# Kernel tuning notes

Measured on AMD Instinct MI355X. Metric: run time of the kernel, lower is better.

Reference implementation:

```python
import jax, jax.numpy as jnp
import numpy as np

N_NODES = 50000
N_EDGES = 800000
IN_CH = 384
HID = 128


def _gcn_conv(x, src, dst, W, b, n):
    # PyG GCNConv: h = x @ W; out[dst] += d^-1/2[src] * d^-1/2[dst] * h[src]; out += b
    h = x @ W  # [N, out_ch]
    deg = jax.ops.segment_sum(jnp.ones(src.shape, dtype=h.dtype), dst, num_segments=n)
    dinv = jnp.where(deg > 0, jax.lax.rsqrt(jnp.maximum(deg, 1.0)), 0.0)
    norm = dinv[src] * dinv[dst]  # [E]
    out = jax.ops.segment_sum(h[src] * norm[:, None], dst, num_segments=n)
    return out + b


def setup_inputs() -> dict:
    key = jax.random.key(0)
    k_x, k_e, k1, k2, k3, k4 = jax.random.split(key, 6)
    x = jax.random.normal(k_x, (N_NODES, IN_CH), dtype=jnp.float32)
    edge_index = jax.random.randint(k_e, (2, N_EDGES), 0, N_NODES, dtype=jnp.int64)
    s1 = 1.0 / np.sqrt(IN_CH)
    s2 = 1.0 / np.sqrt(HID)
    W1 = jax.random.uniform(k1, (IN_CH, HID), jnp.float32, -s1, s1)
    b1 = jnp.zeros((HID,), jnp.float32)
    W2 = jax.random.uniform(k2, (HID, HID), jnp.float32, -s2, s2)
    b2 = jnp.zeros((HID,), jnp.float32)
    return {"x": x, "edge_index": edge_index, "W1": W1, "b1": b1, "W2": W2, "b2": b2}


def reference(x, edge_index, W1, b1, W2, b2):
    n = x.shape[0]
    loops = jnp.arange(n, dtype=edge_index.dtype)
    src = jnp.concatenate([edge_index[0], loops])  # add_self_loops
    dst = jnp.concatenate([edge_index[1], loops])
    h = _gcn_conv(x, src, dst, W1, b1, n)
    h = jax.nn.relu(h)  # dropout is identity in eval mode
    out = _gcn_conv(h, src, dst, W2, b2, n)
    return out
```

## Files before the change

### kernel.cpp

```cpp
#include <hip/hip_runtime.h>
#include <hip/hip_fp16.h>

#define NN 50000
#define NE 800000
#define C_IN 384
#define C_HID 128
#define CHK 128
#define ECH 6250
#define NBKT 128
#define BSTR 392

typedef __attribute__((ext_vector_type(8))) short short8;
typedef __attribute__((ext_vector_type(4))) float f32x4;
typedef __attribute__((ext_vector_type(8))) unsigned short us8;

__device__ __forceinline__ ushort f2bf(float x) {
    uint u = __float_as_uint(x);
    uint r = (u + 0x7fffu + ((u >> 16) & 1u)) >> 16;
    return (ushort)r;
}
__device__ __forceinline__ float bf2f(ushort b) { return __uint_as_float(((uint)b) << 16); }

typedef __attribute__((address_space(1))) const unsigned int as1_uint;
typedef __attribute__((address_space(3))) unsigned int as3_uint;
__device__ __forceinline__ void gload16(const void* g, void* l) {
    __builtin_amdgcn_global_load_lds((as1_uint*)g, (as3_uint*)l, 16, 0, 0);
}

__global__ __launch_bounds__(256) void k_hist(const int* __restrict__ dst,
                                              int* __restrict__ histT) {
    __shared__ int h[NBKT];
    const int tid = threadIdx.x;
    if (tid < NBKT) h[tid] = 0;
    __syncthreads();
    const int base = blockIdx.x * ECH;
    for (int i = base + tid; i < base + ECH; i += 256)
        atomicAdd(&h[(uint)dst[i] / BSTR], 1);
    __syncthreads();
    if (tid < NBKT) histT[tid * CHK + blockIdx.x] = h[tid];
}

__global__ __launch_bounds__(1024) void k_hscan(const int* __restrict__ histT,
                                                int* __restrict__ histS) {
    __shared__ int part[1024];
    const int t = threadIdx.x;
    const int base = t * 16;
    int loc[16];
    int s = 0;
#pragma unroll
    for (int i = 0; i < 16; ++i) {
        loc[i] = histT[base + i];
        s += loc[i];
    }
    part[t] = s;
    __syncthreads();
    for (int off = 1; off < 1024; off <<= 1) {
        int v = (t >= off) ? part[t - off] : 0;
        __syncthreads();
        part[t] += v;
        __syncthreads();
    }
    int run = (t == 0) ? 0 : part[t - 1];
#pragma unroll
    for (int i = 0; i < 16; ++i) {
        histS[base + i] = run;
        run += loc[i];
    }
}

__global__ __launch_bounds__(256) void k_binscat(const int* __restrict__ src,
                                                 const int* __restrict__ dst,
                                                 const int* __restrict__ histS,
                                                 uint2* __restrict__ mid) {
    __shared__ int cur[NBKT];
    const int tid = threadIdx.x;
    if (tid < NBKT) cur[tid] = histS[tid * CHK + blockIdx.x];
    __syncthreads();
    const int base = blockIdx.x * ECH;
    for (int i = base + tid; i < base + ECH; i += 256) {
        const int s = src[i];
        const int d = dst[i];
        const int p = atomicAdd(&cur[(uint)d / BSTR], 1);
        mid[p] = make_uint2((uint)d, (uint)s << 16);
    }
}

__global__ __launch_bounds__(256) void k_bcnt_scan(const uint2* __restrict__ mid,
                                                   const int* __restrict__ histS,
                                                   int* __restrict__ rowptr,
                                                   float* __restrict__ dinv) {
    __shared__ int cur[BSTR];
    __shared__ int part[256];
    const int tid = threadIdx.x;
    const int b = blockIdx.x;
    for (int j = tid; j < BSTR; j += 256) cur[j] = 0;
    __syncthreads();
    const int lo = histS[b * CHK];
    const int hi = (b < NBKT - 1) ? histS[(b + 1) * CHK] : NE;
    for (int e = lo + tid; e < hi; e += 256)
        atomicAdd(&cur[mid[e].x - (uint)b * BSTR], 1);
    __syncthreads();
    const int i0 = 2 * tid;
    const int v0 = (i0 < BSTR) ? cur[i0] : 0;
    const int v1 = (i0 + 1 < BSTR) ? cur[i0 + 1] : 0;
    part[tid] = v0 + v1;
    __syncthreads();
    for (int off = 1; off < 256; off <<= 1) {
        int v = (tid >= off) ? part[tid - off] : 0;
        __syncthreads();
        part[tid] += v;
        __syncthreads();
    }
    const int base = lo + ((tid > 0) ? part[tid - 1] : 0);
    const int idx0 = b * BSTR + i0;
    if (i0 < BSTR && idx0 < NN) {
        rowptr[idx0] = base;
        dinv[idx0] = rsqrtf((float)v0 + 1.0f);
    }
    if (i0 + 1 < BSTR && idx0 + 1 < NN) {
        rowptr[idx0 + 1] = base + v0;
        dinv[idx0 + 1] = rsqrtf((float)v1 + 1.0f);
    }
    if (b == NBKT - 1 && tid == 0) rowptr[NN] = NE;
}

__global__ __launch_bounds__(256) void k_binfill(const uint2* __restrict__ mid,
                                                 const int* __restrict__ histS,
                                                 const int* __restrict__ rowptr,
                                                 const float* __restrict__ dinv,
                                                 uint* __restrict__ csr) {
    __shared__ int cur[BSTR];
    __shared__ float sdv[BSTR];
    const int tid = threadIdx.x;
    const int b = blockIdx.x;
    for (int j = tid; j < BSTR; j += 256) {
        const int idx = b * BSTR + j;
        cur[j] = (idx < NN) ? rowptr[idx] : 0;
        sdv[j] = (idx < NN) ? dinv[idx] : 0.f;
    }
    __syncthreads();
    const int lo = histS[b * CHK];
    const int hi = (b < NBKT - 1) ? histS[(b + 1) * CHK] : NE;
    for (int e = lo + tid; e < hi; e += 256) {
        const uint2 u = mid[e];
        const int j = u.x - (uint)b * BSTR;
        const float norm = dinv[u.y >> 16] * sdv[j];
        const int p = atomicAdd(&cur[j], 1);
        csr[p] = u.y | __half_as_ushort(__float2half(norm));
    }
}

__device__ __forceinline__ void wconv_one(const float* W, ushort* Wt, int i) {
    int k = i >> 7, n = i & 127;
    float w = W[i];
    ushort h = f2bf(w);
    ushort l = f2bf(w - bf2f(h));
    int blk = k >> 5, kq = (k >> 3) & 3, j = k & 7;
    int t = n >> 4, fr = n & 15, lane = kq * 16 + fr;
    size_t off = ((size_t)blk * 1024 + t * 64 + lane) * 8 + j;
    Wt[off] = h;
    Wt[off + 4096] = l;
}

__global__ __launch_bounds__(256) void k_wconv2(const float* __restrict__ W1,
                                                const float* __restrict__ W2,
                                                ushort* __restrict__ Wt1,
                                                ushort* __restrict__ Wt2) {
    int i = blockIdx.x * 256 + threadIdx.x;
    if (i < C_IN * C_HID) {
        wconv_one(W1, Wt1, i);
    } else {
        int j = i - C_IN * C_HID;
        if (j < C_HID * C_HID) wconv_one(W2, Wt2, j);
    }
}

#define STAGE_X(NXT, XOLD, KB1)                                                          \
    {                                                                                    \
        float xs0 = XOLD.x, xs1 = XOLD.y, xs2 = XOLD.z, xs3 = XOLD.w;                    \
        if (IN_RELU_BIAS) {                                                              \
            float4 bq = *(const float4*)(&bias_lds[(KB1) * 32 + (tid & 7) * 4]);         \
            xs0 = fmaxf(xs0 + bq.x, 0.f);                                                \
            xs1 = fmaxf(xs1 + bq.y, 0.f);                                                \
            xs2 = fmaxf(xs2 + bq.z, 0.f);                                                \
            xs3 = fmaxf(xs3 + bq.w, 0.f);                                                \
        }                                                                                \
        const uint u0 = __float_as_uint(xs0), u1 = __float_as_uint(xs1);                 \
        const uint u2 = __float_as_uint(xs2), u3 = __float_as_uint(xs3);                 \
        const uint h01 = (u0 >> 16) | (u1 & 0xffff0000u);                                \
        const uint h23 = (u2 >> 16) | (u3 & 0xffff0000u);                                \
        const uint l0 = __float_as_uint(xs0 - __uint_as_float(u0 & 0xffff0000u));        \
        const uint l1 = __float_as_uint(xs1 - __uint_as_float(u1 & 0xffff0000u));        \
        const uint l2 = __float_as_uint(xs2 - __uint_as_float(u2 & 0xffff0000u));        \
        const uint l3 = __float_as_uint(xs3 - __uint_as_float(u3 & 0xffff0000u));        \
        const uint l01 = (l0 >> 16) | (l1 & 0xffff0000u);                                \
        const uint l23 = (l2 >> 16) | (l3 & 0xffff0000u);                                \
        *(uint2*)&XLh[NXT][xw] = make_uint2(h01, h23);                                   \
        *(uint2*)&XLl[NXT][xw] = make_uint2(l01, l23);                                   \
    }

#define GEMM_BODY(KB, CUR, NXT, XOLD, XNEW)                                              \
    {                                                                                    \
        _Pragma("unroll")                                                                \
        for (int i_ = 0; i_ < 2; ++i_)                                                   \
            gload16(Wt8 + (size_t)((KB) + 1) * 1024 + wv * 128 + i_ * 64 + lane,         \
                    &WL[NXT][wv * 128 + i_ * 64]);                                       \
        __builtin_amdgcn_sched_barrier(0);                                               \
        XNEW = *(const float4*)(xsrc + ((KB) + 2) * 32);                                 \
        const short8 ahh = *(const short8*)&XLh[CUR][axh];                               \
        const short8 all = *(const short8*)&XLl[CUR][axh];                               \
        const short8 wh0 = WL[CUR][(tb + 0) * 64 + lane];                                \
        const short8 wl0 = WL[CUR][512 + (tb + 0) * 64 + lane];                          \
        const short8 wh1 = WL[CUR][(tb + 1) * 64 + lane];                                \
        const short8 wl1 = WL[CUR][512 + (tb + 1) * 64 + lane];                          \
        const short8 wh2 = WL[CUR][(tb + 2) * 64 + lane];                                \
        const short8 wl2 = WL[CUR][512 + (tb + 2) * 64 + lane];                          \
        const short8 wh3 = WL[CUR][(tb + 3) * 64 + lane];                                \
        const short8 wl3 = WL[CUR][512 + (tb + 3) * 64 + lane];                          \
        STAGE_X(NXT, XOLD, (KB) + 1);                                                    \
        __builtin_amdgcn_s_setprio(1);                                                   \
        acc[0] = __builtin_amdgcn_mfma_f32_16x16x32_bf16(ahh, wh0, acc[0], 0, 0, 0);     \
        acc[0] = __builtin_amdgcn_mfma_f32_16x16x32_bf16(ahh, wl0, acc[0], 0, 0, 0);     \
        acc[0] = __builtin_amdgcn_mfma_f32_16x16x32_bf16(all, wh0, acc[0], 0, 0, 0);     \
        acc[1] = __builtin_amdgcn_mfma_f32_16x16x32_bf16(ahh, wh1, acc[1], 0, 0, 0);     \
        acc[1] = __builtin_amdgcn_mfma_f32_16x16x32_bf16(ahh, wl1, acc[1], 0, 0, 0);     \
        acc[1] = __builtin_amdgcn_mfma_f32_16x16x32_bf16(all, wh1, acc[1], 0, 0, 0);     \
        acc[2] = __builtin_amdgcn_mfma_f32_16x16x32_bf16(ahh, wh2, acc[2], 0, 0, 0);     \
        acc[2] = __builtin_amdgcn_mfma_f32_16x16x32_bf16(ahh, wl2, acc[2], 0, 0, 0);     \
        acc[2] = __builtin_amdgcn_mfma_f32_16x16x32_bf16(all, wh2, acc[2], 0, 0, 0);     \
        acc[3] = __builtin_amdgcn_mfma_f32_16x16x32_bf16(ahh, wh3, acc[3], 0, 0, 0);     \
        acc[3] = __builtin_amdgcn_mfma_f32_16x16x32_bf16(ahh, wl3, acc[3], 0, 0, 0);     \
        acc[3] = __builtin_amdgcn_mfma_f32_16x16x32_bf16(all, wh3, acc[3], 0, 0, 0);     \
        __builtin_amdgcn_s_setprio(0);                                                   \
        __builtin_amdgcn_sched_barrier(0);                                               \
        asm volatile("s_waitcnt vmcnt(1) lgkmcnt(0)" ::: "memory");                      \
        __builtin_amdgcn_sched_barrier(0);                                               \
        __builtin_amdgcn_s_barrier();                                                    \
    }

#define GEMM_TAIL(CUR)                                                                   \
    {                                                                                    \
        const short8 ahh = *(const short8*)&XLh[CUR][axh];                               \
        const short8 all = *(const short8*)&XLl[CUR][axh];                               \
        const short8 wh0 = WL[CUR][(tb + 0) * 64 + lane];                                \
        const short8 wl0 = WL[CUR][512 + (tb + 0) * 64 + lane];                          \
        const short8 wh1 = WL[CUR][(tb + 1) * 64 + lane];                                \
        const short8 wl1 = WL[CUR][512 + (tb + 1) * 64 + lane];                          \
        const short8 wh2 = WL[CUR][(tb + 2) * 64 + lane];                                \
        const short8 wl2 = WL[CUR][512 + (tb + 2) * 64 + lane];                          \
        const short8 wh3 = WL[CUR][(tb + 3) * 64 + lane];                                \
        const short8 wl3 = WL[CUR][512 + (tb + 3) * 64 + lane];                          \
        acc[0] = __builtin_amdgcn_mfma_f32_16x16x32_bf16(ahh, wh0, acc[0], 0, 0, 0);     \
        acc[0] = __builtin_amdgcn_mfma_f32_16x16x32_bf16(ahh, wl0, acc[0], 0, 0, 0);     \
        acc[0] = __builtin_amdgcn_mfma_f32_16x16x32_bf16(all, wh0, acc[0], 0, 0, 0);     \
        acc[1] = __builtin_amdgcn_mfma_f32_16x16x32_bf16(ahh, wh1, acc[1], 0, 0, 0);     \
        acc[1] = __builtin_amdgcn_mfma_f32_16x16x32_bf16(ahh, wl1, acc[1], 0, 0, 0);     \
        acc[1] = __builtin_amdgcn_mfma_f32_16x16x32_bf16(all, wh1, acc[1], 0, 0, 0);     \
        acc[2] = __builtin_amdgcn_mfma_f32_16x16x32_bf16(ahh, wh2, acc[2], 0, 0, 0);     \
        acc[2] = __builtin_amdgcn_mfma_f32_16x16x32_bf16(ahh, wl2, acc[2], 0, 0, 0);     \
        acc[2] = __builtin_amdgcn_mfma_f32_16x16x32_bf16(all, wh2, acc[2], 0, 0, 0);     \
        acc[3] = __builtin_amdgcn_mfma_f32_16x16x32_bf16(ahh, wh3, acc[3], 0, 0, 0);     \
        acc[3] = __builtin_amdgcn_mfma_f32_16x16x32_bf16(ahh, wl3, acc[3], 0, 0, 0);     \
        acc[3] = __builtin_amdgcn_mfma_f32_16x16x32_bf16(all, wh3, acc[3], 0, 0, 0);     \
    }

template <bool IN_RELU_BIAS, bool OUT_BIAS>
__global__ __launch_bounds__(512) void k_gemm_mfma(const float* __restrict__ X,
                                                   const ushort* __restrict__ Wt,
                                                   const float* __restrict__ bin,
                                                   const float* __restrict__ bout,
                                                   const float* __restrict__ dinv,
                                                   ushort* __restrict__ out_main,
                                                   float* __restrict__ out_self,
                                                   int K) {
    __shared__ short8 WL[2][1024];
    __shared__ ushort XLh[2][2048];
    __shared__ ushort XLl[2][2048];
    __shared__ float bias_lds[128];

    const int tid = threadIdx.x;
    const int bm = blockIdx.x * 64;
    const int wv = tid >> 6;
    const int lane = tid & 63;
    const int fr = lane & 15;
    const int kq = lane >> 4;
    const int g = wv >> 1;
    const int ch = wv & 1;
    const int tb = ch * 4;
    const int NK = K >> 5;

    const short8* Wt8 = (const short8*)Wt;

    const int xr = tid >> 3;
    const int xc8 = tid & 7;
    int xrow = bm + xr;
    if (xrow >= NN) xrow = NN - 1;
    const float* xsrc = X + (size_t)xrow * K + xc8 * 4;
    const int xw = xr * 32 + (((xc8 >> 1) ^ (xr & 3)) << 3) + ((xc8 & 1) << 2);

    const int ar = g * 16 + fr;
    const int axh = ar * 32 + ((kq ^ (ar & 3)) << 3);

    f32x4 acc[4];
#pragma unroll
    for (int t = 0; t < 4; ++t) acc[t] = (f32x4){0.f, 0.f, 0.f, 0.f};

    if (IN_RELU_BIAS && tid < 128) bias_lds[tid] = bin[tid];

#pragma unroll
    for (int i_ = 0; i_ < 2; ++i_)
        gload16(Wt8 + (size_t)wv * 128 + i_ * 64 + lane, &WL[0][wv * 128 + i_ * 64]);
    __builtin_amdgcn_sched_barrier(0);
    float4 xA = *(const float4*)(xsrc);
    float4 xB = *(const float4*)(xsrc + 32);
    asm volatile("s_waitcnt lgkmcnt(0)" ::: "memory");
    __builtin_amdgcn_s_barrier();
    STAGE_X(0, xA, 0);
    xA = xB;
    asm volatile("s_waitcnt lgkmcnt(0)" ::: "memory");
    __builtin_amdgcn_s_barrier();

    for (int kb = 0; kb < NK - 2; kb += 2) {
        GEMM_BODY(kb, 0, 1, xA, xB);
        GEMM_BODY(kb + 1, 1, 0, xB, xA);
    }

    {
        const int KB = NK - 2;
#pragma unroll
        for (int i_ = 0; i_ < 2; ++i_)
            gload16(Wt8 + (size_t)(KB + 1) * 1024 + wv * 128 + i_ * 64 + lane,
                    &WL[1][wv * 128 + i_ * 64]);
        STAGE_X(1, xA, KB + 1);
        GEMM_TAIL(0);
        __builtin_amdgcn_sched_barrier(0);
        asm volatile("s_waitcnt vmcnt(0) lgkmcnt(0)" ::: "memory");
        __builtin_amdgcn_sched_barrier(0);
        __builtin_amdgcn_s_barrier();
    }
    GEMM_TAIL(1);

#pragma unroll
    for (int r = 0; r < 4; ++r) {
        const int m = bm + g * 16 + kq * 4 + r;
        if (m < NN) {
            const float dv = dinv[m];
            const float d2 = dv * dv;
            ushort* om = out_main + (size_t)m * C_HID;
            float* os = out_self + (size_t)m * C_HID;
#pragma unroll
            for (int t = 0; t < 4; ++t) {
                const int n = (ch * 4 + t) * 16 + fr;
                const float v = acc[t][r];
                om[n] = f2bf(v);
                os[n] = v * d2 + (OUT_BIAS ? bout[n] : 0.f);
            }
        }
    }
}

__global__ __launch_bounds__(256) void k_gather(const ushort* __restrict__ h,
                                                const int* __restrict__ rowptr,
                                                const uint* __restrict__ csr,
                                                float* __restrict__ out) {
    const int tid = threadIdx.x;
    const int node = blockIdx.x * 16 + (tid >> 4);
    if (node >= NN) return;
    const int lane = tid & 15;
    const int c = lane * 8;
    const int beg = rowptr[node];
    const int end = rowptr[node + 1];

    float* op = out + (size_t)node * C_HID + c;
    float4 a0 = *(const float4*)(op);
    float4 a1 = *(const float4*)(op + 4);

    for (int j0 = beg; j0 < end; j0 += 16) {
        const int n = end - j0;
        uint myE = 0;
        if (lane < n) myE = csr[j0 + lane];
        const int m = n < 16 ? n : 16;
        int jj = 0;
        for (; jj + 4 <= m; jj += 4) {
            const uint e0 = (uint)__shfl((int)myE, jj + 0, 16);
            const uint e1 = (uint)__shfl((int)myE, jj + 1, 16);
            const uint e2 = (uint)__shfl((int)myE, jj + 2, 16);
            const uint e3 = (uint)__shfl((int)myE, jj + 3, 16);
            const us8 u0 = *(const us8*)(h + (size_t)(e0 >> 16) * C_HID + c);
            const us8 u1 = *(const us8*)(h + (size_t)(e1 >> 16) * C_HID + c);
            const us8 u2 = *(const us8*)(h + (size_t)(e2 >> 16) * C_HID + c);
            const us8 u3 = *(const us8*)(h + (size_t)(e3 >> 16) * C_HID + c);
            const float n0 = __half2float(__ushort_as_half((ushort)(e0 & 0xffffu)));
            const float n1 = __half2float(__ushort_as_half((ushort)(e1 & 0xffffu)));
            const float n2 = __half2float(__ushort_as_half((ushort)(e2 & 0xffffu)));
            const float n3 = __half2float(__ushort_as_half((ushort)(e3 & 0xffffu)));
            a0.x = fmaf(bf2f(u0[0]), n0, a0.x);
            a0.y = fmaf(bf2f(u0[1]), n0, a0.y);
            a0.z = fmaf(bf2f(u0[2]), n0, a0.z);
            a0.w = fmaf(bf2f(u0[3]), n0, a0.w);
            a1.x = fmaf(bf2f(u0[4]), n0, a1.x);
            a1.y = fmaf(bf2f(u0[5]), n0, a1.y);
            a1.z = fmaf(bf2f(u0[6]), n0, a1.z);
            a1.w = fmaf(bf2f(u0[7]), n0, a1.w);
            a0.x = fmaf(bf2f(u1[0]), n1, a0.x);
            a0.y = fmaf(bf2f(u1[1]), n1, a0.y);
            a0.z = fmaf(bf2f(u1[2]), n1, a0.z);
            a0.w = fmaf(bf2f(u1[3]), n1, a0.w);
            a1.x = fmaf(bf2f(u1[4]), n1, a1.x);
            a1.y = fmaf(bf2f(u1[5]), n1, a1.y);
            a1.z = fmaf(bf2f(u1[6]), n1, a1.z);
            a1.w = fmaf(bf2f(u1[7]), n1, a1.w);
            a0.x = fmaf(bf2f(u2[0]), n2, a0.x);
            a0.y = fmaf(bf2f(u2[1]), n2, a0.y);
            a0.z = fmaf(bf2f(u2[2]), n2, a0.z);
            a0.w = fmaf(bf2f(u2[3]), n2, a0.w);
            a1.x = fmaf(bf2f(u2[4]), n2, a1.x);
            a1.y = fmaf(bf2f(u2[5]), n2, a1.y);
            a1.z = fmaf(bf2f(u2[6]), n2, a1.z);
            a1.w = fmaf(bf2f(u2[7]), n2, a1.w);
            a0.x = fmaf(bf2f(u3[0]), n3, a0.x);
            a0.y = fmaf(bf2f(u3[1]), n3, a0.y);
            a0.z = fmaf(bf2f(u3[2]), n3, a0.z);
            a0.w = fmaf(bf2f(u3[3]), n3, a0.w);
            a1.x = fmaf(bf2f(u3[4]), n3, a1.x);
            a1.y = fmaf(bf2f(u3[5]), n3, a1.y);
            a1.z = fmaf(bf2f(u3[6]), n3, a1.z);
            a1.w = fmaf(bf2f(u3[7]), n3, a1.w);
        }
        for (; jj < m; ++jj) {
            const uint ev = (uint)__shfl((int)myE, jj, 16);
            const us8 u = *(const us8*)(h + (size_t)(ev >> 16) * C_HID + c);
            const float nw = __half2float(__ushort_as_half((ushort)(ev & 0xffffu)));
            a0.x = fmaf(bf2f(u[0]), nw, a0.x);
            a0.y = fmaf(bf2f(u[1]), nw, a0.y);
            a0.z = fmaf(bf2f(u[2]), nw, a0.z);
            a0.w = fmaf(bf2f(u[3]), nw, a0.w);
            a1.x = fmaf(bf2f(u[4]), nw, a1.x);
            a1.y = fmaf(bf2f(u[5]), nw, a1.y);
            a1.z = fmaf(bf2f(u[6]), nw, a1.z);
            a1.w = fmaf(bf2f(u[7]), nw, a1.w);
        }
    }
    *(float4*)(op) = a0;
    *(float4*)(op + 4) = a1;
}

extern "C" void kernel_launch(void* const* d_in, const int* in_sizes, int n_in,
                              void* d_out, int out_size, void* d_ws, size_t ws_size,
                              hipStream_t stream) {
    const float* x = (const float*)d_in[0];
    const int* ei = (const int*)d_in[1];
    const float* W1 = (const float*)d_in[2];
    const float* b1 = (const float*)d_in[3];
    const float* W2 = (const float*)d_in[4];
    const float* b2 = (const float*)d_in[5];
    float* out = (float*)d_out;

    const int* src = ei;
    const int* dst = ei + NE;

    int* cnt = (int*)d_ws;
    int* rowptr = cnt + 50048;
    float* dinv = (float*)(rowptr + 50064);
    int* bsum = (int*)(dinv + 50048);
    int* bpre = bsum + 256;
    int* histT = bpre + 256;
    int* histS = histT + 16384;
    ushort* Wt1 = (ushort*)(histS + 16384);
    ushort* Wt2 = Wt1 + 98304;
    uint* csr = (uint*)(Wt2 + 32768);
    uint2* mid = (uint2*)(csr + NE);
    ushort* A_bf = (ushort*)(mid + NE);
    float* B = (float*)(A_bf + (size_t)NN * C_HID);

    k_wconv2<<<(C_IN * C_HID + C_HID * C_HID + 255) / 256, 256, 0, stream>>>(W1, W2, Wt1, Wt2);
    k_hist<<<CHK, 256, 0, stream>>>(dst, histT);
    k_hscan<<<1, 1024, 0, stream>>>(histT, histS);
    k_binscat<<<CHK, 256, 0, stream>>>(src, dst, histS, mid);
    k_bcnt_scan<<<NBKT, 256, 0, stream>>>(mid, histS, rowptr, dinv);
    k_binfill<<<NBKT, 256, 0, stream>>>(mid, histS, rowptr, dinv, csr);

    const int gblocks = (NN + 63) / 64;
    const int agblocks = (NN + 15) / 16;
    k_gemm_mfma<false, false><<<gblocks, 512, 0, stream>>>(x, Wt1, nullptr, nullptr, dinv, A_bf, B, C_IN);
    k_gather<<<agblocks, 256, 0, stream>>>(A_bf, rowptr, csr, B);
    k_gemm_mfma<true, true><<<gblocks, 512, 0, stream>>>(B, Wt2, b1, b2, dinv, A_bf, out, C_HID);
    k_gather<<<agblocks, 256, 0, stream>>>(A_bf, rowptr, csr, out);
}
```

Baseline: 296.9 us.

## Fuse graph-prep kernels and overlap CSR fill with the first GEMM

Merges the weight conversion and the histogram into one launch, and drops the single-block global scan kernel. Each later block now recomputes the bucket prefix sums from the transposed histogram. The CSR fill is folded into the first MFMA GEMM launch as extra blocks, so it runs alongside the GEMM. This cuts launch count and serial single-block stages, at the cost of redundant prefix-sum work per block and a more complex GEMM kernel that branches on block index.

```diff
diff --git a/kernel.cpp b/kernel.cpp
--- a/kernel.cpp
+++ b/kernel.cpp
@@ -9,6 +9,7 @@
 #define ECH 6250
 #define NBKT 128
 #define BSTR 392
+#define GBLK 782
 
 typedef __attribute__((ext_vector_type(8))) short short8;
 typedef __attribute__((ext_vector_type(4))) float f32x4;
@@ -27,56 +28,75 @@
     __builtin_amdgcn_global_load_lds((as1_uint*)g, (as3_uint*)l, 16, 0, 0);
 }
 
-__global__ __launch_bounds__(256) void k_hist(const int* __restrict__ dst,
-                                              int* __restrict__ histT) {
-    __shared__ int h[NBKT];
+__device__ __forceinline__ void wconv_one(const float* W, ushort* Wt, int i) {
+    int k = i >> 7, n = i & 127;
+    float w = W[i];
+    ushort h = f2bf(w);
+    ushort l = f2bf(w - bf2f(h));
+    int blk = k >> 5, kq = (k >> 3) & 3, j = k & 7;
+    int t = n >> 4, fr = n & 15, lane = kq * 16 + fr;
+    size_t off = ((size_t)blk * 1024 + t * 64 + lane) * 8 + j;
+    Wt[off] = h;
+    Wt[off + 4096] = l;
+}
+
+__global__ __launch_bounds__(256) void k_prep(const int* __restrict__ dst,
+                                              int* __restrict__ histT,
+                                              const float* __restrict__ W1,
+                                              const float* __restrict__ W2,
+                                              ushort* __restrict__ Wt1,
+                                              ushort* __restrict__ Wt2) {
     const int tid = threadIdx.x;
-    if (tid < NBKT) h[tid] = 0;
-    __syncthreads();
-    const int base = blockIdx.x * ECH;
-    for (int i = base + tid; i < base + ECH; i += 256)
-        atomicAdd(&h[(uint)dst[i] / BSTR], 1);
-    __syncthreads();
-    if (tid < NBKT) histT[tid * CHK + blockIdx.x] = h[tid];
-}
-
-__global__ __launch_bounds__(1024) void k_hscan(const int* __restrict__ histT,
-                                                int* __restrict__ histS) {
-    __shared__ int part[1024];
-    const int t = threadIdx.x;
-    const int base = t * 16;
-    int loc[16];
-    int s = 0;
-#pragma unroll
-    for (int i = 0; i < 16; ++i) {
-        loc[i] = histT[base + i];
-        s += loc[i];
-    }
-    part[t] = s;
-    __syncthreads();
-    for (int off = 1; off < 1024; off <<= 1) {
-        int v = (t >= off) ? part[t - off] : 0;
-        __syncthreads();
-        part[t] += v;
-        __syncthreads();
-    }
-    int run = (t == 0) ? 0 : part[t - 1];
-#pragma unroll
-    for (int i = 0; i < 16; ++i) {
-        histS[base + i] = run;
-        run += loc[i];
+    if (blockIdx.x < CHK) {
+        __shared__ int h[NBKT];
+        if (tid < NBKT) h[tid] = 0;
+        __syncthreads();
+        const int base = blockIdx.x * ECH;
+        for (int i = base + tid; i < base + ECH; i += 256)
+            atomicAdd(&h[(uint)dst[i] / BSTR], 1);
+        __syncthreads();
+        if (tid < NBKT) histT[blockIdx.x * NBKT + tid] = h[tid];
+    } else {
+        int i = (blockIdx.x - CHK) * 256 + tid;
+        if (i < C_IN * C_HID) {
+            wconv_one(W1, Wt1, i);
+        } else {
+            int j = i - C_IN * C_HID;
+            if (j < C_HID * C_HID) wconv_one(W2, Wt2, j);
+        }
     }
 }
 
 __global__ __launch_bounds__(256) void k_binscat(const int* __restrict__ src,
                                                  const int* __restrict__ dst,
-                                                 const int* __restrict__ histS,
+                                                 const int* __restrict__ histT,
                                                  uint2* __restrict__ mid) {
     __shared__ int cur[NBKT];
+    __shared__ int sc[NBKT];
     const int tid = threadIdx.x;
-    if (tid < NBKT) cur[tid] = histS[tid * CHK + blockIdx.x];
+    const int myc = blockIdx.x;
+    int tot = 0;
+    if (tid < NBKT) {
+        int part = 0;
+        for (int c = 0; c < CHK; ++c) {
+            int v = histT[c * NBKT + tid];
+            tot += v;
+            if (c < myc) part += v;
+        }
+        sc[tid] = tot;
+        cur[tid] = part;
+    }
     __syncthreads();
-    const int base = blockIdx.x * ECH;
+    for (int off = 1; off < NBKT; off <<= 1) {
+        int v = 0;
+        if (tid < NBKT && tid >= off) v = sc[tid - off];
+        __syncthreads();
+        if (tid < NBKT) sc[tid] += v;
+        __syncthreads();
+    }
+    if (tid < NBKT) cur[tid] += sc[tid] - tot;
+    __syncthreads();
+    const int base = myc * ECH;
     for (int i = base + tid; i < base + ECH; i += 256) {
         const int s = src[i];
         const int d = dst[i];
@@ -86,17 +106,32 @@
 }
 
 __global__ __launch_bounds__(256) void k_bcnt_scan(const uint2* __restrict__ mid,
-                                                   const int* __restrict__ histS,
+                                                   const int* __restrict__ histT,
                                                    int* __restrict__ rowptr,
                                                    float* __restrict__ dinv) {
     __shared__ int cur[BSTR];
     __shared__ int part[256];
+    __shared__ int sc[NBKT];
+    __shared__ int sLO, sHI;
     const int tid = threadIdx.x;
     const int b = blockIdx.x;
     for (int j = tid; j < BSTR; j += 256) cur[j] = 0;
+    int tot = 0;
+    if (tid < NBKT) {
+        for (int c = 0; c < CHK; ++c) tot += histT[c * NBKT + tid];
+        sc[tid] = tot;
+    }
     __syncthreads();
-    const int lo = histS[b * CHK];
-    const int hi = (b < NBKT - 1) ? histS[(b + 1) * CHK] : NE;
+    for (int off = 1; off < NBKT; off <<= 1) {
+        int v = 0;
+        if (tid < NBKT && tid >= off) v = sc[tid - off];
+        __syncthreads();
+        if (tid < NBKT) sc[tid] += v;
+        __syncthreads();
+    }
+    if (tid == b) { sLO = sc[b] - tot; sHI = sc[b]; }
+    __syncthreads();
+    const int lo = sLO, hi = sHI;
     for (int e = lo + tid; e < hi; e += 256)
         atomicAdd(&cur[mid[e].x - (uint)b * BSTR], 1);
     __syncthreads();
@@ -122,57 +157,6 @@
         dinv[idx0 + 1] = rsqrtf((float)v1 + 1.0f);
     }
     if (b == NBKT - 1 && tid == 0) rowptr[NN] = NE;
-}
-
-__global__ __launch_bounds__(256) void k_binfill(const uint2* __restrict__ mid,
-                                                 const int* __restrict__ histS,
-                                                 const int* __restrict__ rowptr,
-                                                 const float* __restrict__ dinv,
-                                                 uint* __restrict__ csr) {
-    __shared__ int cur[BSTR];
-    __shared__ float sdv[BSTR];
-    const int tid = threadIdx.x;
-    const int b = blockIdx.x;
-    for (int j = tid; j < BSTR; j += 256) {
-        const int idx = b * BSTR + j;
-        cur[j] = (idx < NN) ? rowptr[idx] : 0;
-        sdv[j] = (idx < NN) ? dinv[idx] : 0.f;
-    }
-    __syncthreads();
-    const int lo = histS[b * CHK];
-    const int hi = (b < NBKT - 1) ? histS[(b + 1) * CHK] : NE;
-    for (int e = lo + tid; e < hi; e += 256) {
-        const uint2 u = mid[e];
-        const int j = u.x - (uint)b * BSTR;
-        const float norm = dinv[u.y >> 16] * sdv[j];
-        const int p = atomicAdd(&cur[j], 1);
-        csr[p] = u.y | __half_as_ushort(__float2half(norm));
-    }
-}
-
-__device__ __forceinline__ void wconv_one(const float* W, ushort* Wt, int i) {
-    int k = i >> 7, n = i & 127;
-    float w = W[i];
-    ushort h = f2bf(w);
-    ushort l = f2bf(w - bf2f(h));
-    int blk = k >> 5, kq = (k >> 3) & 3, j = k & 7;
-    int t = n >> 4, fr = n & 15, lane = kq * 16 + fr;
-    size_t off = ((size_t)blk * 1024 + t * 64 + lane) * 8 + j;
-    Wt[off] = h;
-    Wt[off + 4096] = l;
-}
-
-__global__ __launch_bounds__(256) void k_wconv2(const float* __restrict__ W1,
-                                                const float* __restrict__ W2,
-                                                ushort* __restrict__ Wt1,
-                                                ushort* __restrict__ Wt2) {
-    int i = blockIdx.x * 256 + threadIdx.x;
-    if (i < C_IN * C_HID) {
-        wconv_one(W1, Wt1, i);
-    } else {
-        int j = i - C_IN * C_HID;
-        if (j < C_HID * C_HID) wconv_one(W2, Wt2, j);
-    }
 }
 
 #define STAGE_X(NXT, XOLD, KB1)                                                          \
@@ -264,7 +248,7 @@
         acc[3] = __builtin_amdgcn_mfma_f32_16x16x32_bf16(all, wh3, acc[3], 0, 0, 0);     \
     }
 
-template <bool IN_RELU_BIAS, bool OUT_BIAS>
+template <bool IN_RELU_BIAS, bool OUT_BIAS, bool FILL>
 __global__ __launch_bounds__(512) void k_gemm_mfma(const float* __restrict__ X,
                                                    const ushort* __restrict__ Wt,
                                                    const float* __restrict__ bin,
@@ -272,13 +256,56 @@
                                                    const float* __restrict__ dinv,
                                                    ushort* __restrict__ out_main,
                                                    float* __restrict__ out_self,
-                                                   int K) {
+                                                   int K,
+                                                   const uint2* __restrict__ mid,
+                                                   const int* __restrict__ histT,
+                                                   const int* __restrict__ rowptr,
+                                                   uint* __restrict__ csr) {
     __shared__ short8 WL[2][1024];
     __shared__ ushort XLh[2][2048];
     __shared__ ushort XLl[2][2048];
     __shared__ float bias_lds[128];
+    __shared__ int sLO, sHI;
 
     const int tid = threadIdx.x;
+
+    if (FILL && blockIdx.x >= GBLK) {
+        const int b = blockIdx.x - GBLK;
+        int* cur = (int*)&WL[0][0];
+        float* sdv = (float*)&WL[0][256];
+        int* sc = (int*)&WL[1][0];
+        int tot = 0;
+        if (tid < NBKT) {
+            for (int c = 0; c < CHK; ++c) tot += histT[c * NBKT + tid];
+            sc[tid] = tot;
+        }
+        __syncthreads();
+        for (int off = 1; off < NBKT; off <<= 1) {
+            int v = 0;
+            if (tid < NBKT && tid >= off) v = sc[tid - off];
+            __syncthreads();
+            if (tid < NBKT) sc[tid] += v;
+            __syncthreads();
+        }
+        if (tid == b) { sLO = sc[b] - tot; sHI = sc[b]; }
+        __syncthreads();
+        const int lo = sLO, hi = sHI;
+        for (int j = tid; j < BSTR; j += 512) {
+            const int idx = b * BSTR + j;
+            cur[j] = (idx < NN) ? rowptr[idx] : 0;
+            sdv[j] = (idx < NN) ? dinv[idx] : 0.f;
+        }
+        __syncthreads();
+        for (int e = lo + tid; e < hi; e += 512) {
+            const uint2 u = mid[e];
+            const int j = u.x - (uint)b * BSTR;
+            const float norm = dinv[u.y >> 16] * sdv[j];
+            const int p = atomicAdd(&cur[j], 1);
+            csr[p] = u.y | __half_as_ushort(__float2half(norm));
+        }
+        return;
+    }
+
     const int bm = blockIdx.x * 64;
     const int wv = tid >> 6;
     const int lane = tid & 63;
@@ -473,17 +500,16 @@
     ushort* A_bf = (ushort*)(mid + NE);
     float* B = (float*)(A_bf + (size_t)NN * C_HID);
 
-    k_wconv2<<<(C_IN * C_HID + C_HID * C_HID + 255) / 256, 256, 0, stream>>>(W1, W2, Wt1, Wt2);
-    k_hist<<<CHK, 256, 0, stream>>>(dst, histT);
-    k_hscan<<<1, 1024, 0, stream>>>(histT, histS);
-    k_binscat<<<CHK, 256, 0, stream>>>(src, dst, histS, mid);
-    k_bcnt_scan<<<NBKT, 256, 0, stream>>>(mid, histS, rowptr, dinv);
-    k_binfill<<<NBKT, 256, 0, stream>>>(mid, histS, rowptr, dinv, csr);
-
-    const int gblocks = (NN + 63) / 64;
+    const int wblocks = (C_IN * C_HID + C_HID * C_HID + 255) / 256;
     const int agblocks = (NN + 15) / 16;
-    k_gemm_mfma<false, false><<<gblocks, 512, 0, stream>>>(x, Wt1, nullptr, nullptr, dinv, A_bf, B, C_IN);
+
+    k_prep<<<CHK + wblocks, 256, 0, stream>>>(dst, histT, W1, W2, Wt1, Wt2);
+    k_binscat<<<CHK, 256, 0, stream>>>(src, dst, histT, mid);
+    k_bcnt_scan<<<NBKT, 256, 0, stream>>>(mid, histT, rowptr, dinv);
+    k_gemm_mfma<false, false, true><<<GBLK + NBKT, 512, 0, stream>>>(
+        x, Wt1, nullptr, nullptr, dinv, A_bf, B, C_IN, mid, histT, rowptr, csr);
     k_gather<<<agblocks, 256, 0, stream>>>(A_bf, rowptr, csr, B);
-    k_gemm_mfma<true, true><<<gblocks, 512, 0, stream>>>(B, Wt2, b1, b2, dinv, A_bf, out, C_HID);
+    k_gemm_mfma<true, true, false><<<GBLK, 512, 0, stream>>>(
+        B, Wt2, b1, b2, dinv, A_bf, out, C_HID, nullptr, nullptr, nullptr, nullptr);
     k_gather<<<agblocks, 256, 0, stream>>>(A_bf, rowptr, csr, out);
 }
```

Measured after the change: 290.1 us. -2.3%, faster.
